# Performance work log

Hardware: AMD Instinct MI355X
Metric: run time of the kernel (lower is better)

The kernel has to match this reference:

```python
import math
import jax, jax.numpy as jnp
import numpy as np

# ---- SLAYER neuron / simulation constants (from config) ----
THETA = 10.0      # spike threshold
TAU_SR = 10.0     # PSP (SRM) kernel time constant
TAU_REF = 1.0     # refractory kernel time constant
TS = 1.0          # simulation time step
T_SAMPLE = 500    # number of time bins
B, N_IN, N_HID, N_OUT = 64, 1024, 1024, 10


def _alpha_kernel(tau, mult, eps=0.01):
    """slayer _calculateAlphaKernel: mult * t/tau * exp(1 - t/tau), truncated."""
    vals = []
    t = 0.0
    while t < T_SAMPLE:
        v = mult * t / tau * math.exp(1.0 - t / tau)
        if abs(v) < eps and t > tau:
            break
        vals.append(v)
        t += TS
    return np.asarray(vals, np.float32)

SRM_KERNEL = jnp.asarray(_alpha_kernel(TAU_SR, 1.0))            # [K]
REF_KERNEL = jnp.asarray(_alpha_kernel(TAU_REF, -2.0 * THETA))  # [Kr], REF_KERNEL[0] == 0


def dense(x, W):
    # per-timestep fully-connected layer (slayer.dense == 1x1x1 conv3d, no bias)
    # x: [B, Nin, T], W: [Nout, Nin] -> [B, Nout, T]
    return jnp.einsum('oi,bit->bot', W, x)


def psp(x):
    # causal temporal convolution with the SRM kernel: out[t] = Ts * sum_k srm[k] * x[t-k]
    Bx, N, T = x.shape
    K = SRM_KERNEL.shape[0]
    k = SRM_KERNEL[::-1].reshape(1, 1, K).astype(x.dtype)  # flip -> true convolution
    y = jax.lax.conv_general_dilated(
        x.reshape(Bx * N, 1, T), k, (1,), [(K - 1, 0)],
        dimension_numbers=('NCH', 'OIH', 'NCH'))
    return y.reshape(Bx, N, T) * TS


def spike_impl(u_in):
    # sequential LIF thresholding with refractory feedback (slayer spike kernel)
    # u_in: [B, N, T] membrane drive; returns (spikes, membrane) both [B, N, T]
    Kr = REF_KERNEL.shape[0]
    # buf[j] is the refractory contribution arriving at step t+j; new spike at t
    # contributes REF_KERNEL[j] at t+j (REF_KERNEL[0]==0), i.e. shifted kernel into buf.
    refk = jnp.concatenate([REF_KERNEL[1:], jnp.zeros((1,), u_in.dtype)]).astype(u_in.dtype)
    buf0 = jnp.zeros(u_in.shape[:-1] + (Kr,), u_in.dtype)

    def step(buf, u_t):
        u = u_t + buf[..., 0]                              # membrane at time t
        s = (u >= THETA).astype(u_in.dtype) / TS           # spike (amplitude 1/Ts)
        buf = jnp.concatenate([buf[..., 1:], jnp.zeros_like(buf[..., :1])], axis=-1)
        buf = buf + s[..., None] * refk
        return buf, (s, u)

    _, (s, u) = jax.lax.scan(step, buf0, jnp.moveaxis(u_in, -1, 0))
    return jnp.moveaxis(s, 0, -1), jnp.moveaxis(u, 0, -1)


def setup_inputs() -> dict:
    key = jax.random.key(0)
    k1, k2, k3 = jax.random.split(key, 3)
    spike_input = (jax.random.uniform(k1, (B, N_IN, T_SAMPLE)) < 0.05).astype(jnp.float32)
    W1 = jax.random.normal(k2, (N_HID, N_IN), jnp.float32) * 0.3
    W2 = jax.random.normal(k3, (N_OUT, N_HID), jnp.float32) * 0.3
    return {"spike_input": spike_input, "W1": W1, "W2": W2}


def reference(spike_input, W1, W2):
    s1, _ = spike_impl(psp(dense(spike_input, W1)))
    s2, _ = spike_impl(psp(dense(s1, W2)))
    return s2
```

## Files before the change

### kernel.cpp

```cpp
#include <hip/hip_runtime.h>
#include <stdint.h>
#include <math.h>

#define T_SIM 500
#define NB    64
#define NIN   1024
#define NHID  1024
#define NOUT  10
#define KSRM  77
#define CHUNK 32
#define TT3   16
#define NT3   32
#define RING3 108

__device__ __forceinline__ double srm_tap(int k) {
  double u = (double)k / 10.0;
  double v = u * exp(1.0 - u);
  return (double)(float)v;
}
__device__ __forceinline__ double ref_tap(int j) {
  double v = (-20.0 * (double)j) * exp(1.0 - (double)j);
  return (double)(float)v;
}

__global__ __launch_bounds__(64)
void k_pack(const float* __restrict__ x, unsigned long long* __restrict__ bits) {
  const int b = blockIdx.x, ig = blockIdx.y, tc = blockIdx.z;
  const int lane = threadIdx.x;
  const float* xr = x + ((size_t)b * NIN + ig * 64 + lane) * T_SIM;
  const int t0 = tc * 100;
  for (int t = t0; t < t0 + 100; t += 4) {
    const float4 v = *(const float4*)(xr + t);
    unsigned long long m0 = __ballot(v.x > 0.5f);
    unsigned long long m1 = __ballot(v.y > 0.5f);
    unsigned long long m2 = __ballot(v.z > 0.5f);
    unsigned long long m3 = __ballot(v.w > 0.5f);
    if (lane == 0) {
      unsigned long long* w = bits + (size_t)(b * T_SIM + t) * 16 + ig;
      w[0] = m0; w[16] = m1; w[32] = m2; w[48] = m3;
    }
  }
}

__global__ __launch_bounds__(256)
void k_transpose(const float* __restrict__ W1, float* __restrict__ W1T) {
  __shared__ float tile[64][65];
  const int bo = blockIdx.x * 64, bi = blockIdx.y * 64;
  for (int k = threadIdx.x; k < 4096; k += 256) {
    int r = k >> 6, c = k & 63;
    tile[r][c] = W1[(size_t)(bo + r) * NIN + bi + c];
  }
  __syncthreads();
  for (int k = threadIdx.x; k < 4096; k += 256) {
    int r = k >> 6, c = k & 63;
    W1T[(size_t)(bi + r) * NHID + bo + c] = tile[c][r];
  }
}

__global__ __launch_bounds__(128)
void k_dense1(const uint32_t* __restrict__ bits, const float* __restrict__ W1T,
              double* __restrict__ a1c, int col_base) {
  __shared__ int list[NIN];
  __shared__ int nact_s;
  const int col_loc = blockIdx.x;
  const int tid = threadIdx.x;
  if (tid < 32) {
    uint32_t w = bits[(size_t)(col_base + col_loc) * 32 + tid];
    int c = __popc(w);
    int p = c;
#pragma unroll
    for (int d = 1; d < 32; d <<= 1) {
      int q = __shfl_up(p, d);
      if (tid >= d) p += q;
    }
    int excl = p - c;
    while (w) {
      const int j = __ffs(w) - 1;
      w &= w - 1;
      list[excl++] = tid * 32 + j;
    }
    if (tid == 31) nact_s = excl;
  }
  __syncthreads();
  const int n = nact_s;
  const int o = blockIdx.y * 512 + tid * 4;
  double a0x=0,a0y=0,a0z=0,a0w=0, a1x=0,a1y=0,a1z=0,a1w=0;
  double a2x=0,a2y=0,a2z=0,a2w=0, a3x=0,a3y=0,a3z=0,a3w=0;
  float4 L0, L1, L2, L3;
  int g = 0;
  if (g + 4 <= n) {
    L0 = *(const float4*)(W1T + (size_t)list[0] * NHID + o);
    L1 = *(const float4*)(W1T + (size_t)list[1] * NHID + o);
    L2 = *(const float4*)(W1T + (size_t)list[2] * NHID + o);
    L3 = *(const float4*)(W1T + (size_t)list[3] * NHID + o);
  }
  for (; g + 4 <= n; g += 4) {
    float4 N0, N1, N2, N3;
    const bool more = (g + 8 <= n);
    if (more) {
      N0 = *(const float4*)(W1T + (size_t)list[g+4] * NHID + o);
      N1 = *(const float4*)(W1T + (size_t)list[g+5] * NHID + o);
      N2 = *(const float4*)(W1T + (size_t)list[g+6] * NHID + o);
      N3 = *(const float4*)(W1T + (size_t)list[g+7] * NHID + o);
    }
    a0x += (double)L0.x; a0y += (double)L0.y; a0z += (double)L0.z; a0w += (double)L0.w;
    a1x += (double)L1.x; a1y += (double)L1.y; a1z += (double)L1.z; a1w += (double)L1.w;
    a2x += (double)L2.x; a2y += (double)L2.y; a2z += (double)L2.z; a2w += (double)L2.w;
    a3x += (double)L3.x; a3y += (double)L3.y; a3z += (double)L3.z; a3w += (double)L3.w;
    if (more) { L0 = N0; L1 = N1; L2 = N2; L3 = N3; }
  }
  if (g + 0 < n) {
    const float4 wv = *(const float4*)(W1T + (size_t)list[g+0] * NHID + o);
    a0x += (double)wv.x; a0y += (double)wv.y; a0z += (double)wv.z; a0w += (double)wv.w;
  }
  if (g + 1 < n) {
    const float4 wv = *(const float4*)(W1T + (size_t)list[g+1] * NHID + o);
    a1x += (double)wv.x; a1y += (double)wv.y; a1z += (double)wv.z; a1w += (double)wv.w;
  }
  if (g + 2 < n) {
    const float4 wv = *(const float4*)(W1T + (size_t)list[g+2] * NHID + o);
    a2x += (double)wv.x; a2y += (double)wv.y; a2z += (double)wv.z; a2w += (double)wv.w;
  }
  double4 r;
  r.x = (a0x + a1x) + (a2x + a3x);
  r.y = (a0y + a1y) + (a2y + a3y);
  r.z = (a0z + a1z) + (a2z + a3z);
  r.w = (a0w + a1w) + (a2w + a3w);
  *(double4*)(a1c + (size_t)col_loc * NHID + o) = r;
}

__global__ __launch_bounds__(512)
void k_ps1(const double* __restrict__ a1c, uint32_t* __restrict__ s1w,
           int b_base) {
  __shared__ double S[RING3 * 32];
  __shared__ double Y[4][TT3 * 32];
  __shared__ double TB[80];
  const int ng = blockIdx.x, b_loc = blockIdx.y;
  const int tid = threadIdx.x;

  const double* __restrict__ abase = a1c + (size_t)b_loc * T_SIM * NHID + ng * 32;
  uint32_t* __restrict__ sbase = s1w + (size_t)(b_base + b_loc) * T_SIM * 32 + ng;

  if (tid < 80) TB[tid] = (tid <= 76) ? srm_tap(tid) : 0.0;
  for (int i = tid; i < RING3 * 32; i += 512) S[i] = 0.0;
  __syncthreads();
  for (int id = tid; id < TT3 * 32; id += 512) {
    const int r = id >> 5, nn = id & 31;
    S[r * 32 + nn] = abase[(size_t)r * NHID + nn];
  }

  const int g  = tid >> 7;
  const int tq = (tid >> 5) & 3;
  const int n  = tid & 31;
  double tap[20];
  __syncthreads();
#pragma unroll
  for (int j = 0; j < 20; ++j) tap[j] = TB[20 * g + j];

  double refk[11];
#pragma unroll
  for (int j = 1; j <= 10; ++j) refk[j] = ref_tap(j);
  uint32_t smask = 0;

  for (int k = 0; k < NT3; ++k) {
    const int t0 = k * TT3;
    const int tv = (T_SIM - t0 < TT3) ? (T_SIM - t0) : TT3;
    {
      const int tb = t0 + tq * 4;
      int slot = tb - 20 * g - 19;
      slot %= RING3; if (slot < 0) slot += RING3;
      double a0 = 0, a1 = 0, a2 = 0, a3 = 0;
#pragma unroll
      for (int s = 0; s < 23; ++s) {
        const double v = S[slot * 32 + n];
        slot = (slot + 1 == RING3) ? 0 : slot + 1;
        if (s <= 19)            a0 += tap[19 - s] * v;
        if (s >= 1 && s <= 20)  a1 += tap[20 - s] * v;
        if (s >= 2 && s <= 21)  a2 += tap[21 - s] * v;
        if (s >= 3)             a3 += tap[22 - s] * v;
      }
      double* Yg = Y[g];
      const int tl = tq * 4;
      Yg[(tl + 0) * 32 + n] = a0;
      Yg[(tl + 1) * 32 + n] = a1;
      Yg[(tl + 2) * 32 + n] = a2;
      Yg[(tl + 3) * 32 + n] = a3;
    }
    __syncthreads();
    const int t0n = t0 + TT3;
    const int tvn = (t0n >= T_SIM) ? 0 : ((T_SIM - t0n < TT3) ? (T_SIM - t0n) : TT3);
    if (tid < 32) {
      for (int gg = 0; gg < tv; ++gg) {
        double u = (Y[0][gg * 32 + tid] + Y[1][gg * 32 + tid]) +
                   (Y[2][gg * 32 + tid] + Y[3][gg * 32 + tid]);
#pragma unroll
        for (int j = 10; j >= 1; --j)
          u += refk[j] * (double)((smask >> (j - 1)) & 1u);
        const bool sp = (u >= 10.0);
        smask = (smask << 1) | (sp ? 1u : 0u);
        const unsigned long long bm = __ballot(sp);
        if (tid == 0) sbase[(size_t)(t0 + gg) * 32] = (uint32_t)bm;
      }
    } else if (tid >= 64) {
      for (int id = tid - 64; id < tvn * 32; id += 448) {
        const int r = id >> 5, nn = id & 31;
        S[((t0n + r) % RING3) * 32 + nn] = abase[(size_t)(t0n + r) * NHID + nn];
      }
    }
    __syncthreads();
  }
}

__global__ __launch_bounds__(256)
void k_dense2(const uint32_t* __restrict__ s1w,
              const float* __restrict__ W2, double* __restrict__ a2) {
  __shared__ float w2t[NHID * NOUT];
  for (int k = threadIdx.x; k < NHID * NOUT; k += 256) {
    const int o = k >> 10, i = k & 1023;
    w2t[i * NOUT + o] = W2[k];
  }
  __syncthreads();
  const int col = blockIdx.x * 256 + threadIdx.x;
  double acc[NOUT];
#pragma unroll
  for (int o = 0; o < NOUT; ++o) acc[o] = 0.0;
  const uint32_t* w = s1w + (size_t)col * 32;
  for (int wi = 0; wi < 32; ++wi) {
    uint32_t m = w[wi];
    const int ibase = wi * 32;
    while (m) {
      const int j = __ffs(m) - 1;
      m &= m - 1;
      const float* row = &w2t[(ibase + j) * NOUT];
#pragma unroll
      for (int o = 0; o < NOUT; ++o) acc[o] += (double)row[o];
    }
  }
  double* outp = a2 + (size_t)col * NOUT;
#pragma unroll
  for (int o = 0; o < NOUT; ++o) outp[o] = acc[o];
}

__global__ __launch_bounds__(256)
void k_l2(const double* __restrict__ a2, float* __restrict__ out) {
  __shared__ double S[T_SIM * NOUT];
  __shared__ double Y[T_SIM * NOUT];
  __shared__ double srm[KSRM];
  const int b = blockIdx.x, tid = threadIdx.x;
  if (tid < KSRM) srm[tid] = srm_tap(tid);
  for (int i = tid; i < T_SIM * NOUT; i += 256)
    S[i] = a2[(size_t)b * T_SIM * NOUT + i];
  __syncthreads();
  for (int i = tid; i < T_SIM * NOUT; i += 256) {
    const int t = i / 10, o = i - t * 10;
    const int kmax = (t < KSRM - 1) ? t : (KSRM - 1);
    double acc = 0.0;
    for (int k = 0; k <= kmax; ++k)
      acc += srm[k] * S[(t - k) * 10 + o];
    Y[i] = acc;
  }
  __syncthreads();
  if (tid < NOUT) {
    double refk[11];
#pragma unroll
    for (int j = 1; j <= 10; ++j) refk[j] = ref_tap(j);
    uint32_t smask = 0;
    float* op = out + ((size_t)b * NOUT + tid) * T_SIM;
    for (int t = 0; t < T_SIM; ++t) {
      double u = Y[t * 10 + tid];
#pragma unroll
      for (int j = 10; j >= 1; --j)
        u += refk[j] * (double)((smask >> (j - 1)) & 1u);
      const bool sp = (u >= 10.0);
      smask = (smask << 1) | (sp ? 1u : 0u);
      op[t] = sp ? 1.0f : 0.0f;
    }
  }
}

extern "C" void kernel_launch(void* const* d_in, const int* in_sizes, int n_in,
                              void* d_out, int out_size, void* d_ws, size_t ws_size,
                              hipStream_t stream) {
  const float* x  = (const float*)d_in[0];
  const float* W1 = (const float*)d_in[1];
  const float* W2 = (const float*)d_in[2];
  float* out = (float*)d_out;

  char* ws = (char*)d_ws;
  unsigned long long* bits1 = (unsigned long long*)(ws);
  float*  W1T = (float*) (ws + 4096000);
  double* a1c = (double*)(ws + 8290304);
  uint32_t* s1w = (uint32_t*)(ws + 139362304);
  double* a2  = (double*)(ws + 143458304);

  hipLaunchKernelGGL(k_pack, dim3(NB, 16, 5), dim3(64), 0, stream, x, bits1);
  hipLaunchKernelGGL(k_transpose, dim3(16, 16), dim3(256), 0, stream, W1, W1T);

  for (int bc = 0; bc < NB; bc += CHUNK) {
    hipLaunchKernelGGL(k_dense1, dim3(CHUNK * T_SIM, 2), dim3(128), 0, stream,
                       (const uint32_t*)bits1, W1T, a1c, bc * T_SIM);
    hipLaunchKernelGGL(k_ps1, dim3(32, CHUNK), dim3(512), 0, stream,
                       a1c, s1w, bc);
  }

  hipLaunchKernelGGL(k_dense2, dim3(125), dim3(256), 0, stream, s1w, W2, a2);
  hipLaunchKernelGGL(k_l2, dim3(NB), dim3(256), 0, stream, a2, out);
}
```

Measured before the change: 1.012 ms.

## Pipeline PSP FIR with spike scan via double-buffered tiles and deepen dense1 prefetch

k_ps1 now gives the FIR convolution to 384 threads and the sequential spike scan to a separate wavefront. The scan runs on the previous tile's double-buffered outputs while the FIR computes the next tile, so each tile needs one barrier instead of two. The ring buffer becomes a power of two so modulo becomes masking, and prefetch of the next input tile is folded into the FIR threads. k_dense1 prefetches 8 weight rows per step instead of 4 and uses nontemporal stores. The cost is more registers and a more complex schedule.

```diff
diff --git a/kernel.cpp b/kernel.cpp
--- a/kernel.cpp
+++ b/kernel.cpp
@@ -9,9 +9,9 @@
 #define NOUT  10
 #define KSRM  77
 #define CHUNK 32
-#define TT3   16
-#define NT3   32
-#define RING3 108
+#define TT5   12
+#define NT5   42
+#define RING5 128
 
 __device__ __forceinline__ double srm_tap(int k) {
   double u = (double)k / 10.0;
@@ -84,130 +84,157 @@
   __syncthreads();
   const int n = nact_s;
   const int o = blockIdx.y * 512 + tid * 4;
-  double a0x=0,a0y=0,a0z=0,a0w=0, a1x=0,a1y=0,a1z=0,a1w=0;
-  double a2x=0,a2y=0,a2z=0,a2w=0, a3x=0,a3y=0,a3z=0,a3w=0;
-  float4 L0, L1, L2, L3;
+  double ax[4] = {0,0,0,0}, ay[4] = {0,0,0,0};
+  double az[4] = {0,0,0,0}, aw[4] = {0,0,0,0};
+  float4 L[8];
   int g = 0;
-  if (g + 4 <= n) {
-    L0 = *(const float4*)(W1T + (size_t)list[0] * NHID + o);
-    L1 = *(const float4*)(W1T + (size_t)list[1] * NHID + o);
-    L2 = *(const float4*)(W1T + (size_t)list[2] * NHID + o);
-    L3 = *(const float4*)(W1T + (size_t)list[3] * NHID + o);
-  }
-  for (; g + 4 <= n; g += 4) {
-    float4 N0, N1, N2, N3;
-    const bool more = (g + 8 <= n);
-    if (more) {
-      N0 = *(const float4*)(W1T + (size_t)list[g+4] * NHID + o);
-      N1 = *(const float4*)(W1T + (size_t)list[g+5] * NHID + o);
-      N2 = *(const float4*)(W1T + (size_t)list[g+6] * NHID + o);
-      N3 = *(const float4*)(W1T + (size_t)list[g+7] * NHID + o);
-    }
-    a0x += (double)L0.x; a0y += (double)L0.y; a0z += (double)L0.z; a0w += (double)L0.w;
-    a1x += (double)L1.x; a1y += (double)L1.y; a1z += (double)L1.z; a1w += (double)L1.w;
-    a2x += (double)L2.x; a2y += (double)L2.y; a2z += (double)L2.z; a2w += (double)L2.w;
-    a3x += (double)L3.x; a3y += (double)L3.y; a3z += (double)L3.z; a3w += (double)L3.w;
-    if (more) { L0 = N0; L1 = N1; L2 = N2; L3 = N3; }
-  }
-  if (g + 0 < n) {
-    const float4 wv = *(const float4*)(W1T + (size_t)list[g+0] * NHID + o);
-    a0x += (double)wv.x; a0y += (double)wv.y; a0z += (double)wv.z; a0w += (double)wv.w;
-  }
-  if (g + 1 < n) {
-    const float4 wv = *(const float4*)(W1T + (size_t)list[g+1] * NHID + o);
-    a1x += (double)wv.x; a1y += (double)wv.y; a1z += (double)wv.z; a1w += (double)wv.w;
-  }
-  if (g + 2 < n) {
-    const float4 wv = *(const float4*)(W1T + (size_t)list[g+2] * NHID + o);
-    a2x += (double)wv.x; a2y += (double)wv.y; a2z += (double)wv.z; a2w += (double)wv.w;
-  }
-  double4 r;
-  r.x = (a0x + a1x) + (a2x + a3x);
-  r.y = (a0y + a1y) + (a2y + a3y);
-  r.z = (a0z + a1z) + (a2z + a3z);
-  r.w = (a0w + a1w) + (a2w + a3w);
-  *(double4*)(a1c + (size_t)col_loc * NHID + o) = r;
-}
-
-__global__ __launch_bounds__(512)
+  if (n >= 8) {
+#pragma unroll
+    for (int r = 0; r < 8; ++r)
+      L[r] = *(const float4*)(W1T + (size_t)list[r] * NHID + o);
+    for (g = 0; g + 16 <= n; g += 8) {
+      float4 Nb[8];
+#pragma unroll
+      for (int r = 0; r < 8; ++r)
+        Nb[r] = *(const float4*)(W1T + (size_t)list[g + 8 + r] * NHID + o);
+#pragma unroll
+      for (int r = 0; r < 8; ++r) {
+        const int s = r & 3;
+        ax[s] += (double)L[r].x; ay[s] += (double)L[r].y;
+        az[s] += (double)L[r].z; aw[s] += (double)L[r].w;
+      }
+#pragma unroll
+      for (int r = 0; r < 8; ++r) L[r] = Nb[r];
+    }
+#pragma unroll
+    for (int r = 0; r < 8; ++r) {
+      const int s = r & 3;
+      ax[s] += (double)L[r].x; ay[s] += (double)L[r].y;
+      az[s] += (double)L[r].z; aw[s] += (double)L[r].w;
+    }
+    g += 8;
+  }
+  for (; g < n; ++g) {
+    const float4 wv = *(const float4*)(W1T + (size_t)list[g] * NHID + o);
+    const int s = g & 3;
+    ax[s] += (double)wv.x; ay[s] += (double)wv.y;
+    az[s] += (double)wv.z; aw[s] += (double)wv.w;
+  }
+  double* dst = a1c + (size_t)col_loc * NHID + o;
+  __builtin_nontemporal_store((ax[0] + ax[1]) + (ax[2] + ax[3]), dst + 0);
+  __builtin_nontemporal_store((ay[0] + ay[1]) + (ay[2] + ay[3]), dst + 1);
+  __builtin_nontemporal_store((az[0] + az[1]) + (az[2] + az[3]), dst + 2);
+  __builtin_nontemporal_store((aw[0] + aw[1]) + (aw[2] + aw[3]), dst + 3);
+}
+
+__global__ __launch_bounds__(448)
 void k_ps1(const double* __restrict__ a1c, uint32_t* __restrict__ s1w,
            int b_base) {
-  __shared__ double S[RING3 * 32];
-  __shared__ double Y[4][TT3 * 32];
+  __shared__ double S[RING5 * 32];
+  __shared__ double Yp[2][4][TT5 * 32];
   __shared__ double TB[80];
   const int ng = blockIdx.x, b_loc = blockIdx.y;
   const int tid = threadIdx.x;
-
   const double* __restrict__ abase = a1c + (size_t)b_loc * T_SIM * NHID + ng * 32;
   uint32_t* __restrict__ sbase = s1w + (size_t)(b_base + b_loc) * T_SIM * 32 + ng;
 
   if (tid < 80) TB[tid] = (tid <= 76) ? srm_tap(tid) : 0.0;
-  for (int i = tid; i < RING3 * 32; i += 512) S[i] = 0.0;
-  __syncthreads();
-  for (int id = tid; id < TT3 * 32; id += 512) {
+  for (int i = tid; i < RING5 * 32; i += 448) S[i] = 0.0;
+  __syncthreads();
+  for (int id = tid; id < TT5 * 32; id += 448) {
     const int r = id >> 5, nn = id & 31;
     S[r * 32 + nn] = abase[(size_t)r * NHID + nn];
   }
 
-  const int g  = tid >> 7;
-  const int tq = (tid >> 5) & 3;
-  const int n  = tid & 31;
+  const bool isFIR = (tid < 384);
+  const int g   = tid / 96;
+  const int rem = tid - g * 96;
+  const int q   = rem >> 5;
+  const int n   = rem & 31;
   double tap[20];
   __syncthreads();
-#pragma unroll
-  for (int j = 0; j < 20; ++j) tap[j] = TB[20 * g + j];
-
+  if (isFIR) {
+#pragma unroll
+    for (int j = 0; j < 20; ++j) tap[j] = TB[20 * g + j];
+  }
   double refk[11];
 #pragma unroll
   for (int j = 1; j <= 10; ++j) refk[j] = ref_tap(j);
   uint32_t smask = 0;
 
-  for (int k = 0; k < NT3; ++k) {
-    const int t0 = k * TT3;
-    const int tv = (T_SIM - t0 < TT3) ? (T_SIM - t0) : TT3;
-    {
-      const int tb = t0 + tq * 4;
-      int slot = tb - 20 * g - 19;
-      slot %= RING3; if (slot < 0) slot += RING3;
+  for (int k = 0; k < NT5; ++k) {
+    const int t0 = k * TT5;
+    const int tv = (T_SIM - t0 < TT5) ? (T_SIM - t0) : TT5;
+    const int t0n = t0 + TT5;
+    const int tvn = (t0n >= T_SIM) ? 0 : ((T_SIM - t0n < TT5) ? (T_SIM - t0n) : TT5);
+    if (isFIR) {
+      double pf = 0.0;
+      const int pr = tid >> 5, pn = tid & 31;
+      const bool hasPf = (tid < tvn * 32);
+      if (hasPf) pf = abase[(size_t)(t0n + pr) * NHID + pn];
+      const int tb = t0 + q * 4;
+      int slot = (tb - 20 * g - 19 + 1024) & (RING5 - 1);
       double a0 = 0, a1 = 0, a2 = 0, a3 = 0;
 #pragma unroll
       for (int s = 0; s < 23; ++s) {
         const double v = S[slot * 32 + n];
-        slot = (slot + 1 == RING3) ? 0 : slot + 1;
-        if (s <= 19)            a0 += tap[19 - s] * v;
-        if (s >= 1 && s <= 20)  a1 += tap[20 - s] * v;
-        if (s >= 2 && s <= 21)  a2 += tap[21 - s] * v;
-        if (s >= 3)             a3 += tap[22 - s] * v;
+        slot = (slot + 1) & (RING5 - 1);
+        if (s <= 19)           a0 += tap[19 - s] * v;
+        if (s >= 1 && s <= 20) a1 += tap[20 - s] * v;
+        if (s >= 2 && s <= 21) a2 += tap[21 - s] * v;
+        if (s >= 3)            a3 += tap[22 - s] * v;
       }
-      double* Yg = Y[g];
-      const int tl = tq * 4;
-      Yg[(tl + 0) * 32 + n] = a0;
-      Yg[(tl + 1) * 32 + n] = a1;
-      Yg[(tl + 2) * 32 + n] = a2;
-      Yg[(tl + 3) * 32 + n] = a3;
+      double* Yk = Yp[k & 1][g];
+      const int tl = q * 4;
+      if (tl + 0 < tv) Yk[(tl + 0) * 32 + n] = a0;
+      if (tl + 1 < tv) Yk[(tl + 1) * 32 + n] = a1;
+      if (tl + 2 < tv) Yk[(tl + 2) * 32 + n] = a2;
+      if (tl + 3 < tv) Yk[(tl + 3) * 32 + n] = a3;
+      if (hasPf) S[((t0n + pr) & (RING5 - 1)) * 32 + pn] = pf;
+    } else if (k > 0) {
+      const int lane = tid - 384;
+      if (lane < 32) {
+        const int t0p = t0 - TT5;
+        const double* Y0 = Yp[(k - 1) & 1][0];
+        const double* Y1 = Yp[(k - 1) & 1][1];
+        const double* Y2 = Yp[(k - 1) & 1][2];
+        const double* Y3 = Yp[(k - 1) & 1][3];
+        for (int gg = 0; gg < TT5; ++gg) {
+          double u = (Y0[gg * 32 + lane] + Y1[gg * 32 + lane]) +
+                     (Y2[gg * 32 + lane] + Y3[gg * 32 + lane]);
+#pragma unroll
+          for (int j = 10; j >= 1; --j)
+            u += refk[j] * (double)((smask >> (j - 1)) & 1u);
+          const bool sp = (u >= 10.0);
+          smask = (smask << 1) | (sp ? 1u : 0u);
+          const unsigned long long bm = __ballot(sp);
+          if (lane == 0) sbase[(size_t)(t0p + gg) * 32] = (uint32_t)bm;
+        }
+      }
     }
     __syncthreads();
-    const int t0n = t0 + TT3;
-    const int tvn = (t0n >= T_SIM) ? 0 : ((T_SIM - t0n < TT3) ? (T_SIM - t0n) : TT3);
-    if (tid < 32) {
-      for (int gg = 0; gg < tv; ++gg) {
-        double u = (Y[0][gg * 32 + tid] + Y[1][gg * 32 + tid]) +
-                   (Y[2][gg * 32 + tid] + Y[3][gg * 32 + tid]);
+  }
+  if (!isFIR) {
+    const int lane = tid - 384;
+    if (lane < 32) {
+      const int t0p = (NT5 - 1) * TT5;
+      const int tvp = T_SIM - t0p;
+      const double* Y0 = Yp[(NT5 - 1) & 1][0];
+      const double* Y1 = Yp[(NT5 - 1) & 1][1];
+      const double* Y2 = Yp[(NT5 - 1) & 1][2];
+      const double* Y3 = Yp[(NT5 - 1) & 1][3];
+      for (int gg = 0; gg < tvp; ++gg) {
+        double u = (Y0[gg * 32 + lane] + Y1[gg * 32 + lane]) +
+                   (Y2[gg * 32 + lane] + Y3[gg * 32 + lane]);
 #pragma unroll
         for (int j = 10; j >= 1; --j)
           u += refk[j] * (double)((smask >> (j - 1)) & 1u);
         const bool sp = (u >= 10.0);
         smask = (smask << 1) | (sp ? 1u : 0u);
         const unsigned long long bm = __ballot(sp);
-        if (tid == 0) sbase[(size_t)(t0 + gg) * 32] = (uint32_t)bm;
+        if (lane == 0) sbase[(size_t)(t0p + gg) * 32] = (uint32_t)bm;
       }
-    } else if (tid >= 64) {
-      for (int id = tid - 64; id < tvn * 32; id += 448) {
-        const int r = id >> 5, nn = id & 31;
-        S[((t0n + r) % RING3) * 32 + nn] = abase[(size_t)(t0n + r) * NHID + nn];
-      }
-    }
-    __syncthreads();
+    }
   }
 }
 
@@ -299,7 +326,7 @@
   for (int bc = 0; bc < NB; bc += CHUNK) {
     hipLaunchKernelGGL(k_dense1, dim3(CHUNK * T_SIM, 2), dim3(128), 0, stream,
                        (const uint32_t*)bits1, W1T, a1c, bc * T_SIM);
-    hipLaunchKernelGGL(k_ps1, dim3(32, CHUNK), dim3(512), 0, stream,
+    hipLaunchKernelGGL(k_ps1, dim3(32, CHUNK), dim3(448), 0, stream,
                        a1c, s1w, bc);
   }
 
```

After: 935.4 us. 1.08x faster.
